# Optimization experiments

Measured on AMD Instinct MI355X. Metric: run time of the kernel, lower is better.

## Reference

```python
import jax, jax.numpy as jnp
import numpy as np

B, N = 2048, 100            # batch, n_atoms
NC2 = N * (N - 1) // 2      # 4950 strictly-lower-triangle pairs

# Row-major strictly-lower-triangle indices: (1,0),(2,0),(2,1),(3,0),...
# This matches tf.where over band_part(index_matrix,-1,0)-diag in Triangle.
_TRIL_R, _TRIL_C = np.tril_indices(N, k=-1)


def setup_inputs() -> dict:
    key = jax.random.key(0)
    k1, k2 = jax.random.split(key)
    coords = jax.random.normal(k1, (B, N, 3), dtype=jnp.float32)
    decompFE_flat = jax.random.normal(k2, (B, NC2), dtype=jnp.float32)
    return {"coords": coords, "decompFE_flat": decompFE_flat}


def _triangle(flat):
    """[B, NC2] -> symmetric [B, N, N] with zero diagonal (Q + Q^T)."""
    b = flat.shape[0]
    m = jnp.zeros((b, N, N), dtype=flat.dtype).at[:, _TRIL_R, _TRIL_C].set(flat)
    return m + jnp.swapaxes(m, 1, 2)


def reference(coords, decompFE_flat):
    # Symmetric decomposed pairwise energies [B, N, N]
    decompFE = _triangle(decompFE_flat)

    # Pairwise squared distances [B, N, N]
    diff = coords[:, :, None, :] - coords[:, None, :, :]
    diff2 = jnp.sum(diff * diff, axis=-1)

    # Strictly-lower-triangle distances in row-major order [B, NC2]
    # (TF extracts nonzeros of the lower band; off-diagonal distances are
    #  nonzero for generic coords, so this is exactly the strict lower tri.)
    r_flat = jnp.sqrt(diff2[:, _TRIL_R, _TRIL_C])
    recip_r_flat = 1.0 / r_flat

    # Symmetric 1/r matrix, then einsum 'bijk,bij->bk' with k=1 == full ij sum
    Q3 = _triangle(recip_r_flat)
    E = jnp.sum(Q3 * decompFE, axis=(1, 2), keepdims=True)[:, :, 0] / 2.0  # [B,1]
    return E
```

## Files before the change

kernel.cpp:

```cpp
#include <hip/hip_runtime.h>


#define BATCH 2048
#define NATOMS 100
#define NPAIRS 4950
#define NF2    (NPAIRS / 2)
#define BLOCK 256
#define NWAVES (BLOCK / 64)

__global__ __launch_bounds__(BLOCK) void eij_kernel(
    const float* __restrict__ coords,
    const float* __restrict__ decomp,
    float* __restrict__ out)
{
    __shared__ float sx[NATOMS], sy[NATOMS], sz[NATOMS];
    __shared__ alignas(16) float recip[NPAIRS];
    __shared__ float wave_sums[NWAVES];

    const int b = blockIdx.x;
    const int t = threadIdx.x;
    const int wave = t >> 6;
    const int lane = t & 63;

    const float* cb = coords + (size_t)b * NATOMS * 3;
    for (int a = t; a < NATOMS; a += BLOCK) {
        sx[a] = cb[a * 3 + 0];
        sy[a] = cb[a * 3 + 1];
        sz[a] = cb[a * 3 + 2];
    }
    __syncthreads();

    const int j1 = (lane + 64 < NATOMS) ? (lane + 64) : (NATOMS - 1);
    const float x0 = sx[lane], y0 = sy[lane], z0 = sz[lane];
    const float x1 = sx[j1],   y1 = sy[j1],   z1 = sz[j1];

    for (int i = wave + 1; i < NATOMS; i += NWAVES) {
        const int base = i * (i - 1) / 2;
        const float cix = sx[i];
        const float ciy = sy[i];
        const float ciz = sz[i];

        if (lane < i) {
            const float dx = cix - x0, dy = ciy - y0, dz = ciz - z0;
            recip[base + lane] = rsqrtf(dx * dx + dy * dy + dz * dz);
        }
        if (lane + 64 < i) {
            const float dx = cix - x1, dy = ciy - y1, dz = ciz - z1;
            recip[base + 64 + lane] = rsqrtf(dx * dx + dy * dy + dz * dz);
        }
    }
    __syncthreads();

    const float2* __restrict__ d2 =
        (const float2*)(decomp + (size_t)b * NPAIRS);
    const float2* __restrict__ r2 = (const float2*)recip;

    float acc = 0.0f;
    #pragma unroll
    for (int c = 0; c < (NF2 + BLOCK - 1) / BLOCK; ++c) {
        const int idx = t + c * BLOCK;
        if (idx < NF2) {
            const float2 d = d2[idx];
            const float2 r = r2[idx];
            acc += d.x * r.x + d.y * r.y;
        }
    }

    #pragma unroll
    for (int off = 32; off > 0; off >>= 1)
        acc += __shfl_down(acc, off, 64);
    if (lane == 0) wave_sums[wave] = acc;
    __syncthreads();

    if (t == 0)
        out[b] = wave_sums[0] + wave_sums[1] + wave_sums[2] + wave_sums[3];
}

extern "C" void kernel_launch(void* const* d_in, const int* in_sizes, int n_in,
                              void* d_out, int out_size, void* d_ws, size_t ws_size,
                              hipStream_t stream) {
    const float* coords = (const float*)d_in[0];
    const float* decomp = (const float*)d_in[1];
    float* out = (float*)d_out;

    eij_kernel<<<BATCH, BLOCK, 0, stream>>>(coords, decomp, out);
}
```

Before: 87.11 us.

## Prefetch decomp into registers before distance compute and vectorize coord load

The decomp row is now loaded into registers at kernel start, so its global-memory latency overlaps the shared-memory distance computation instead of following it. Coordinates are staged with float4 loads into one interleaved shared array. This raises register pressure (ten float2 per thread) and may cut occupancy.

```diff
diff --git a/kernel.cpp b/kernel.cpp
--- a/kernel.cpp
+++ b/kernel.cpp
@@ -7,13 +7,14 @@
 #define NF2    (NPAIRS / 2)
 #define BLOCK 256
 #define NWAVES (BLOCK / 64)
+#define NCHUNK ((NF2 + BLOCK - 1) / BLOCK)
 
 __global__ __launch_bounds__(BLOCK) void eij_kernel(
     const float* __restrict__ coords,
     const float* __restrict__ decomp,
     float* __restrict__ out)
 {
-    __shared__ float sx[NATOMS], sy[NATOMS], sz[NATOMS];
+    __shared__ alignas(16) float sc[NATOMS * 3];
     __shared__ alignas(16) float recip[NPAIRS];
     __shared__ float wave_sums[NWAVES];
 
@@ -22,23 +23,32 @@
     const int wave = t >> 6;
     const int lane = t & 63;
 
-    const float* cb = coords + (size_t)b * NATOMS * 3;
-    for (int a = t; a < NATOMS; a += BLOCK) {
-        sx[a] = cb[a * 3 + 0];
-        sy[a] = cb[a * 3 + 1];
-        sz[a] = cb[a * 3 + 2];
+    const float4* __restrict__ cb4 =
+        (const float4*)(coords + (size_t)b * NATOMS * 3);
+    if (t < NATOMS * 3 / 4) ((float4*)sc)[t] = cb4[t];
+
+    const float2* __restrict__ d2 =
+        (const float2*)(decomp + (size_t)b * NPAIRS);
+    float2 dreg[NCHUNK];
+    #pragma unroll
+    for (int c = 0; c < NCHUNK - 1; ++c)
+        dreg[c] = d2[t + c * BLOCK];
+    {
+        const int idx = t + (NCHUNK - 1) * BLOCK;
+        dreg[NCHUNK - 1] = d2[idx < NF2 ? idx : NF2 - 1];
     }
+
     __syncthreads();
 
     const int j1 = (lane + 64 < NATOMS) ? (lane + 64) : (NATOMS - 1);
-    const float x0 = sx[lane], y0 = sy[lane], z0 = sz[lane];
-    const float x1 = sx[j1],   y1 = sy[j1],   z1 = sz[j1];
+    const float x0 = sc[lane * 3 + 0], y0 = sc[lane * 3 + 1], z0 = sc[lane * 3 + 2];
+    const float x1 = sc[j1 * 3 + 0],   y1 = sc[j1 * 3 + 1],   z1 = sc[j1 * 3 + 2];
 
     for (int i = wave + 1; i < NATOMS; i += NWAVES) {
         const int base = i * (i - 1) / 2;
-        const float cix = sx[i];
-        const float ciy = sy[i];
-        const float ciz = sz[i];
+        const float cix = sc[i * 3 + 0];
+        const float ciy = sc[i * 3 + 1];
+        const float ciz = sc[i * 3 + 2];
 
         if (lane < i) {
             const float dx = cix - x0, dy = ciy - y0, dz = ciz - z0;
@@ -51,18 +61,18 @@
     }
     __syncthreads();
 
-    const float2* __restrict__ d2 =
-        (const float2*)(decomp + (size_t)b * NPAIRS);
     const float2* __restrict__ r2 = (const float2*)recip;
-
     float acc = 0.0f;
     #pragma unroll
-    for (int c = 0; c < (NF2 + BLOCK - 1) / BLOCK; ++c) {
-        const int idx = t + c * BLOCK;
+    for (int c = 0; c < NCHUNK - 1; ++c) {
+        const float2 r = r2[t + c * BLOCK];
+        acc += dreg[c].x * r.x + dreg[c].y * r.y;
+    }
+    {
+        const int idx = t + (NCHUNK - 1) * BLOCK;
         if (idx < NF2) {
-            const float2 d = d2[idx];
             const float2 r = r2[idx];
-            acc += d.x * r.x + d.y * r.y;
+            acc += dreg[NCHUNK - 1].x * r.x + dreg[NCHUNK - 1].y * r.y;
         }
     }
 
```

Result: no change. 86.77 us (-0.4%).
